# Kernel tuning notes

Hardware: AMD Instinct MI355X
Metric: run time of the kernel (lower is better)

The kernel has to match this reference:

```python
import jax, jax.numpy as jnp
import numpy as np

GAMMA = 0.5
K = 3
SKIP_THRESHOLD = 1.0


def setup_inputs() -> dict:
    key = jax.random.key(0)
    ks = jax.random.split(key, 11)
    in_dim, out_dim, mem_len = 1024, 128, 131072
    inp = {
        "x": jax.random.normal(ks[0], (1, in_dim), jnp.float32),
        "mean": jax.random.normal(ks[1], (in_dim,), jnp.float32),
        "std": jax.random.uniform(ks[2], (in_dim,), jnp.float32, 0.5, 1.5),
        "memory": jax.random.normal(ks[3], (mem_len, out_dim), jnp.float32),
        "mem_data": jax.random.normal(ks[4], (mem_len, in_dim), jnp.float32),
        "W_enc": jax.random.normal(ks[5], (in_dim, out_dim), jnp.float32) * 0.02,
        "b_enc": jnp.zeros((out_dim,), jnp.float32),
        "W_dec": jax.random.normal(ks[6], (out_dim, in_dim), jnp.float32) * 0.02,
        "b_dec": jnp.zeros((in_dim,), jnp.float32),
        "win_mean": jnp.zeros((), jnp.float32),   # WindowLoss running mean
        "win_std": jnp.ones((), jnp.float32),     # WindowLoss sample std (1 if population_std==0)
    }
    return inp


def reference(x, mean, std, memory, mem_data, W_enc, b_enc, W_dec, b_dec, win_mean, win_std):
    # normalize: new = (x - mean) / std, zero where std == 0
    new = jnp.where(std == 0, 0.0, (x - mean) / std)            # [1, in_dim]
    # encoder: Linear + Tanh
    enc = jnp.tanh(new @ W_enc + b_enc)                          # [1, out_dim]
    # window_loss: decoder reconstruction MSE, gated by ndtr of z-scored loss
    rec = enc @ W_dec + b_dec                                    # [1, in_dim]
    mse = jnp.mean((rec - new) ** 2)                             # scalar
    prob = jax.scipy.special.ndtr((mse - win_mean) / win_std)    # torch uses loss.item() -> constant
    win_loss = (SKIP_THRESHOLD - prob) / SKIP_THRESHOLD * mse
    # L1-distance top-k (smallest) against the memory bank
    dist = jnp.sum(jnp.abs(memory - enc), axis=1)                # [mem_len]
    neg_d, idx = jax.lax.top_k(-dist, K)
    distances = -neg_d                                           # [K] smallest distances
    expw = GAMMA ** jnp.arange(K, dtype=jnp.float32)
    loss_values = jnp.sum(distances * expw) / jnp.sum(expw)
    # conditional FIFO scatter update at the nearest index
    cond = loss_values <= win_loss
    i0 = idx[0]
    new_memory = jnp.where(cond, memory.at[i0].set(enc[0]), memory)
    new_mem_data = jnp.where(cond, mem_data.at[i0].set(x[0]), mem_data)
    loss_combined = win_loss + loss_values
    return loss_combined, new_memory, new_mem_data
```

## Files before the change

### kernel.cpp

```cpp
#include <hip/hip_runtime.h>
#include <math.h>
#include <float.h>

#define IN_DIM   1024
#define OUT_DIM  128
#define MEM_LEN  131072
#define DIST_BLOCKS 2048
#define COPY_BLOCKS 8192

#define NA_FLOATS  ((long long)MEM_LEN * OUT_DIM)
#define NB_FLOATS  ((long long)MEM_LEN * IN_DIM)
#define N_TOTAL    (NA_FLOATS + NB_FLOATS)
#define NA_CHUNKS  (NA_FLOATS / 4)
#define CMAX       ((N_TOTAL - 4) / 4)

__device__ __forceinline__ void ins3(float v, int i,
    float& v0, int& i0, float& v1, int& i1, float& v2, int& i2) {
  if (v < v0 || (v == v0 && i < i0)) {
    v2 = v1; i2 = i1; v1 = v0; i1 = i0; v0 = v; i0 = i;
  } else if (v < v1 || (v == v1 && i < i1)) {
    v2 = v1; i2 = i1; v1 = v; i1 = i;
  } else if (v < v2 || (v == v2 && i < i2)) {
    v2 = v; i2 = i;
  }
}

__global__ __launch_bounds__(1024) void k1_encode(
    const float* __restrict__ x, const float* __restrict__ mean,
    const float* __restrict__ stdv, const float* __restrict__ W_enc,
    const float* __restrict__ b_enc, const float* __restrict__ W_dec,
    const float* __restrict__ b_dec, const float* __restrict__ win_mean,
    const float* __restrict__ win_std,
    float* __restrict__ ws_enc, float* __restrict__ ws_winloss) {
  __shared__ float s_new[IN_DIM];
  __shared__ float s_part[8][OUT_DIM];
  __shared__ float s_enc[OUT_DIM];
  __shared__ float s_red[16];
  const int t = threadIdx.x;
  const float sd = stdv[t];
  const float nv = (sd == 0.0f) ? 0.0f : (x[t] - mean[t]) / sd;
  s_new[t] = nv;
  __syncthreads();
  const int o = t & (OUT_DIM - 1);
  const int p = t >> 7;
  float partial = 0.0f;
  #pragma unroll 8
  for (int i = 0; i < 128; ++i) {
    const int k = p * 128 + i;
    partial += s_new[k] * W_enc[k * OUT_DIM + o];
  }
  s_part[p][o] = partial;
  __syncthreads();
  if (t < OUT_DIM) {
    float sum = b_enc[t];
    #pragma unroll
    for (int pp = 0; pp < 8; ++pp) sum += s_part[pp][t];
    const float e = tanhf(sum);
    s_enc[t] = e;
    ws_enc[t] = e;
  }
  __syncthreads();
  float r = b_dec[t];
  #pragma unroll 8
  for (int k = 0; k < OUT_DIM; ++k) r += s_enc[k] * W_dec[k * IN_DIM + t];
  const float diff = r - nv;
  float sq = diff * diff;
  for (int off = 32; off; off >>= 1) sq += __shfl_xor(sq, off, 64);
  const int lane = t & 63, wid = t >> 6;
  if (lane == 0) s_red[wid] = sq;
  __syncthreads();
  if (t == 0) {
    float tot = 0.0f;
    #pragma unroll
    for (int w = 0; w < 16; ++w) tot += s_red[w];
    const float mse = tot / (float)IN_DIM;
    const float z = (mse - win_mean[0]) / win_std[0];
    const float prob = 0.5f * erfcf(-z * 0.70710678118654752440f);
    ws_winloss[0] = (1.0f - prob) * mse;
  }
}

__global__ __launch_bounds__(256) void k2_dist(
    const float* __restrict__ memory, const float* __restrict__ ws_enc,
    float* __restrict__ topv, int* __restrict__ topi) {
  const int t = threadIdx.x;
  const int lane = t & 63;
  const int wid = t >> 6;
  const int gw = blockIdx.x * 4 + wid;
  const float2 e = reinterpret_cast<const float2*>(ws_enc)[lane];
  float v0 = FLT_MAX, v1 = FLT_MAX, v2 = FLT_MAX;
  int i0 = 0x7fffffff, i1 = 0x7fffffff, i2 = 0x7fffffff;
  const int r0 = gw * 16;
  for (int rr = 0; rr < 16; ++rr) {
    const int r = r0 + rr;
    const float2 m = reinterpret_cast<const float2*>(memory)[(size_t)r * 64 + lane];
    float d = fabsf(m.x - e.x) + fabsf(m.y - e.y);
    for (int off = 32; off; off >>= 1) d += __shfl_xor(d, off, 64);
    ins3(d, r, v0, i0, v1, i1, v2, i2);
  }
  __shared__ float sv[4][3];
  __shared__ int   si[4][3];
  if (lane == 0) {
    sv[wid][0] = v0; sv[wid][1] = v1; sv[wid][2] = v2;
    si[wid][0] = i0; si[wid][1] = i1; si[wid][2] = i2;
  }
  __syncthreads();
  if (t == 0) {
    for (int w = 1; w < 4; ++w)
      for (int j = 0; j < 3; ++j)
        ins3(sv[w][j], si[w][j], v0, i0, v1, i1, v2, i2);
    topv[blockIdx.x * 3 + 0] = v0; topi[blockIdx.x * 3 + 0] = i0;
    topv[blockIdx.x * 3 + 1] = v1; topi[blockIdx.x * 3 + 1] = i1;
    topv[blockIdx.x * 3 + 2] = v2; topi[blockIdx.x * 3 + 2] = i2;
  }
}

__global__ __launch_bounds__(256) void copy_all(
    const float4* __restrict__ mem4, const float4* __restrict__ md4,
    float* __restrict__ out) {
  const int lane = threadIdx.x & 63;
  const int wid  = threadIdx.x >> 6;
  const long long wstride = (long long)gridDim.x * 4;
  const long long ngroups = (CMAX + 63) / 64;
  const float* memf = reinterpret_cast<const float*>(mem4);
  const float* mdf  = reinterpret_cast<const float*>(md4);
  for (long long g = (long long)blockIdx.x * 4 + wid; g < ngroups; g += wstride) {
    const long long c = 1 + g * 64 + lane;
    const bool valid = (c <= CMAX);
    float4 v = make_float4(0.f, 0.f, 0.f, 0.f);
    if (valid) v = (c < NA_CHUNKS) ? mem4[c] : md4[c - NA_CHUNKS];
    float aw = __shfl_up(v.w, 1, 64);
    if (lane == 0) {
      const long long s = 4 * c - 1;
      aw = (s < NA_FLOATS) ? memf[s] : mdf[s - NA_FLOATS];
    }
    if (valid) {
      const float4 o = make_float4(aw, v.x, v.y, v.z);
      *reinterpret_cast<float4*>(out + 4 * c) = o;
    }
  }
  if (blockIdx.x == 0 && threadIdx.x == 0) {
    out[1] = memf[0]; out[2] = memf[1]; out[3] = memf[2];
    out[N_TOTAL] = mdf[NB_FLOATS - 1];
  }
}

__global__ __launch_bounds__(1024) void k3_topk_update(
    const float* __restrict__ topv, const int* __restrict__ topi,
    const float* __restrict__ ws_winloss, const float* __restrict__ ws_enc,
    const float* __restrict__ x, float* __restrict__ out_loss,
    float* __restrict__ out_mem, float* __restrict__ out_md) {
  const int t = threadIdx.x;
  const int n = DIST_BLOCKS * 3;
  float v0 = FLT_MAX, v1 = FLT_MAX, v2 = FLT_MAX;
  int i0 = 0x7fffffff, i1 = 0x7fffffff, i2 = 0x7fffffff;
  for (int j = t; j < n; j += 1024) ins3(topv[j], topi[j], v0, i0, v1, i1, v2, i2);
  for (int off = 32; off; off >>= 1) {
    const float ov0 = __shfl_xor(v0, off, 64);
    const float ov1 = __shfl_xor(v1, off, 64);
    const float ov2 = __shfl_xor(v2, off, 64);
    const int oi0 = __shfl_xor(i0, off, 64);
    const int oi1 = __shfl_xor(i1, off, 64);
    const int oi2 = __shfl_xor(i2, off, 64);
    ins3(ov0, oi0, v0, i0, v1, i1, v2, i2);
    ins3(ov1, oi1, v0, i0, v1, i1, v2, i2);
    ins3(ov2, oi2, v0, i0, v1, i1, v2, i2);
  }
  __shared__ float sv[16][3];
  __shared__ int   si[16][3];
  __shared__ int s_i0, s_cond;
  const int lane = t & 63, wid = t >> 6;
  if (lane == 0) {
    sv[wid][0] = v0; sv[wid][1] = v1; sv[wid][2] = v2;
    si[wid][0] = i0; si[wid][1] = i1; si[wid][2] = i2;
  }
  __syncthreads();
  if (t == 0) {
    for (int w = 1; w < 16; ++w)
      for (int j = 0; j < 3; ++j)
        ins3(sv[w][j], si[w][j], v0, i0, v1, i1, v2, i2);
    const float loss_values = (v0 + 0.5f * v1 + 0.25f * v2) / 1.75f;
    const float wl = ws_winloss[0];
    out_loss[0] = wl + loss_values;
    s_i0 = i0;
    s_cond = (loss_values <= wl) ? 1 : 0;
  }
  __syncthreads();
  if (s_cond) {
    if (t < OUT_DIM) out_mem[(size_t)s_i0 * OUT_DIM + t] = ws_enc[t];
    out_md[(size_t)s_i0 * IN_DIM + t] = x[t];
  }
}

extern "C" void kernel_launch(void* const* d_in, const int* in_sizes, int n_in,
                              void* d_out, int out_size, void* d_ws, size_t ws_size,
                              hipStream_t stream) {
  const float* x        = (const float*)d_in[0];
  const float* mean     = (const float*)d_in[1];
  const float* stdv     = (const float*)d_in[2];
  const float* memory   = (const float*)d_in[3];
  const float* mem_data = (const float*)d_in[4];
  const float* W_enc    = (const float*)d_in[5];
  const float* b_enc    = (const float*)d_in[6];
  const float* W_dec    = (const float*)d_in[7];
  const float* b_dec    = (const float*)d_in[8];
  const float* win_mean = (const float*)d_in[9];
  const float* win_std  = (const float*)d_in[10];

  float* out      = (float*)d_out;
  float* out_loss = out;
  float* out_mem  = out + 1;
  float* out_md   = out + 1 + (size_t)MEM_LEN * OUT_DIM;

  float* ws        = (float*)d_ws;
  float* ws_enc    = ws;
  float* ws_wl     = ws + 128;
  float* ws_topv   = ws + 256;
  int*   ws_topi   = (int*)(ws + 256 + DIST_BLOCKS * 3);

  k1_encode<<<1, 1024, 0, stream>>>(x, mean, stdv, W_enc, b_enc, W_dec, b_dec,
                                    win_mean, win_std, ws_enc, ws_wl);
  k2_dist<<<DIST_BLOCKS, 256, 0, stream>>>(memory, ws_enc, ws_topv, ws_topi);
  copy_all<<<COPY_BLOCKS, 256, 0, stream>>>((const float4*)memory,
                                            (const float4*)mem_data, out);
  k3_topk_update<<<1, 1024, 0, stream>>>(ws_topv, ws_topi, ws_wl, ws_enc, x,
                                         out_loss, out_mem, out_md);
}
```

Baseline: 357.0 us.

## Fuse distance top-k into copy kernel and widen per-lane copy to four float4s

Merges the L1-distance/top-k kernel into the bulk output copy kernel. The first 2048 blocks compute partial top-3 before joining the grid-stride copy, which removes one launch and lets the memory reads of both phases overlap. The copy loop now handles four float4 chunks per lane with a fast path that avoids per-element bounds and source checks, and a slow path only for the group that straddles the two arrays and for the last group. This adds code complexity and makes the first blocks unbalanced relative to the rest.

```diff
diff --git a/kernel.cpp b/kernel.cpp
--- a/kernel.cpp
+++ b/kernel.cpp
@@ -5,14 +5,16 @@
 #define IN_DIM   1024
 #define OUT_DIM  128
 #define MEM_LEN  131072
+#define GRID     8192
 #define DIST_BLOCKS 2048
-#define COPY_BLOCKS 8192
 
 #define NA_FLOATS  ((long long)MEM_LEN * OUT_DIM)
 #define NB_FLOATS  ((long long)MEM_LEN * IN_DIM)
 #define N_TOTAL    (NA_FLOATS + NB_FLOATS)
 #define NA_CHUNKS  (NA_FLOATS / 4)
 #define CMAX       ((N_TOTAL - 4) / 4)
+#define NGROUPS    ((CMAX + 255) / 256)
+#define STRADDLE_G 16383
 
 __device__ __forceinline__ void ins3(float v, int i,
     float& v0, int& i0, float& v1, int& i1, float& v2, int& i2) {
@@ -80,68 +82,92 @@
   }
 }
 
-__global__ __launch_bounds__(256) void k2_dist(
-    const float* __restrict__ memory, const float* __restrict__ ws_enc,
+__global__ __launch_bounds__(256) void k2_fused(
+    const float* __restrict__ memory, const float* __restrict__ mem_data,
+    const float* __restrict__ ws_enc, float* __restrict__ out,
     float* __restrict__ topv, int* __restrict__ topi) {
   const int t = threadIdx.x;
   const int lane = t & 63;
-  const int wid = t >> 6;
-  const int gw = blockIdx.x * 4 + wid;
-  const float2 e = reinterpret_cast<const float2*>(ws_enc)[lane];
-  float v0 = FLT_MAX, v1 = FLT_MAX, v2 = FLT_MAX;
-  int i0 = 0x7fffffff, i1 = 0x7fffffff, i2 = 0x7fffffff;
-  const int r0 = gw * 16;
-  for (int rr = 0; rr < 16; ++rr) {
-    const int r = r0 + rr;
-    const float2 m = reinterpret_cast<const float2*>(memory)[(size_t)r * 64 + lane];
-    float d = fabsf(m.x - e.x) + fabsf(m.y - e.y);
-    for (int off = 32; off; off >>= 1) d += __shfl_xor(d, off, 64);
-    ins3(d, r, v0, i0, v1, i1, v2, i2);
-  }
-  __shared__ float sv[4][3];
-  __shared__ int   si[4][3];
-  if (lane == 0) {
-    sv[wid][0] = v0; sv[wid][1] = v1; sv[wid][2] = v2;
-    si[wid][0] = i0; si[wid][1] = i1; si[wid][2] = i2;
-  }
-  __syncthreads();
-  if (t == 0) {
-    for (int w = 1; w < 4; ++w)
-      for (int j = 0; j < 3; ++j)
-        ins3(sv[w][j], si[w][j], v0, i0, v1, i1, v2, i2);
-    topv[blockIdx.x * 3 + 0] = v0; topi[blockIdx.x * 3 + 0] = i0;
-    topv[blockIdx.x * 3 + 1] = v1; topi[blockIdx.x * 3 + 1] = i1;
-    topv[blockIdx.x * 3 + 2] = v2; topi[blockIdx.x * 3 + 2] = i2;
-  }
-}
-
-__global__ __launch_bounds__(256) void copy_all(
-    const float4* __restrict__ mem4, const float4* __restrict__ md4,
-    float* __restrict__ out) {
-  const int lane = threadIdx.x & 63;
-  const int wid  = threadIdx.x >> 6;
-  const long long wstride = (long long)gridDim.x * 4;
-  const long long ngroups = (CMAX + 63) / 64;
-  const float* memf = reinterpret_cast<const float*>(mem4);
-  const float* mdf  = reinterpret_cast<const float*>(md4);
-  for (long long g = (long long)blockIdx.x * 4 + wid; g < ngroups; g += wstride) {
-    const long long c = 1 + g * 64 + lane;
-    const bool valid = (c <= CMAX);
-    float4 v = make_float4(0.f, 0.f, 0.f, 0.f);
-    if (valid) v = (c < NA_CHUNKS) ? mem4[c] : md4[c - NA_CHUNKS];
-    float aw = __shfl_up(v.w, 1, 64);
+  const int wid  = t >> 6;
+  const float4* mem4 = reinterpret_cast<const float4*>(memory);
+  const float4* md4  = reinterpret_cast<const float4*>(mem_data);
+
+  if (blockIdx.x < DIST_BLOCKS) {
+    const float2 e = reinterpret_cast<const float2*>(ws_enc)[lane];
+    float v0 = FLT_MAX, v1 = FLT_MAX, v2 = FLT_MAX;
+    int i0 = 0x7fffffff, i1 = 0x7fffffff, i2 = 0x7fffffff;
+    const int r0 = (blockIdx.x * 4 + wid) * 16;
+    for (int rr = 0; rr < 16; ++rr) {
+      const int r = r0 + rr;
+      const float2 m = reinterpret_cast<const float2*>(memory)[(size_t)r * 64 + lane];
+      float d = fabsf(m.x - e.x) + fabsf(m.y - e.y);
+      for (int off = 32; off; off >>= 1) d += __shfl_xor(d, off, 64);
+      ins3(d, r, v0, i0, v1, i1, v2, i2);
+    }
+    __shared__ float sv[4][3];
+    __shared__ int   si[4][3];
     if (lane == 0) {
-      const long long s = 4 * c - 1;
-      aw = (s < NA_FLOATS) ? memf[s] : mdf[s - NA_FLOATS];
-    }
-    if (valid) {
-      const float4 o = make_float4(aw, v.x, v.y, v.z);
-      *reinterpret_cast<float4*>(out + 4 * c) = o;
-    }
-  }
-  if (blockIdx.x == 0 && threadIdx.x == 0) {
-    out[1] = memf[0]; out[2] = memf[1]; out[3] = memf[2];
-    out[N_TOTAL] = mdf[NB_FLOATS - 1];
+      sv[wid][0] = v0; sv[wid][1] = v1; sv[wid][2] = v2;
+      si[wid][0] = i0; si[wid][1] = i1; si[wid][2] = i2;
+    }
+    __syncthreads();
+    if (t == 0) {
+      for (int w = 1; w < 4; ++w)
+        for (int j = 0; j < 3; ++j)
+          ins3(sv[w][j], si[w][j], v0, i0, v1, i1, v2, i2);
+      topv[blockIdx.x * 3 + 0] = v0; topi[blockIdx.x * 3 + 0] = i0;
+      topv[blockIdx.x * 3 + 1] = v1; topi[blockIdx.x * 3 + 1] = i1;
+      topv[blockIdx.x * 3 + 2] = v2; topi[blockIdx.x * 3 + 2] = i2;
+    }
+  }
+
+  for (long long g = (long long)blockIdx.x * 4 + wid; g < NGROUPS;
+       g += (long long)GRID * 4) {
+    const long long b = g * 256 + (long long)lane * 4;
+    if (g != STRADDLE_G && g < NGROUPS - 1) {
+      const float4* src = (g < STRADDLE_G) ? mem4 : (md4 - NA_CHUNKS);
+      const float4 a0 = src[b + 1];
+      const float4 a1 = src[b + 2];
+      const float4 a2 = src[b + 3];
+      const float4 a3 = src[b + 4];
+      float prev = __shfl_up(a3.w, 1, 64);
+      if (lane == 0) {
+        const long long s = 1024LL * g + 3;
+        prev = (s < NA_FLOATS) ? memory[s] : mem_data[s - NA_FLOATS];
+      }
+      float4* o4 = reinterpret_cast<float4*>(out + 4 * b + 4);
+      o4[0] = make_float4(prev, a0.x, a0.y, a0.z);
+      o4[1] = make_float4(a0.w, a1.x, a1.y, a1.z);
+      o4[2] = make_float4(a1.w, a2.x, a2.y, a2.z);
+      o4[3] = make_float4(a2.w, a3.x, a3.y, a3.z);
+    } else {
+      float4 av[4];
+      #pragma unroll
+      for (int m = 0; m < 4; ++m) {
+        const long long c = b + 1 + m;
+        av[m] = (c <= CMAX)
+                  ? ((c < NA_CHUNKS) ? mem4[c] : md4[c - NA_CHUNKS])
+                  : make_float4(0.f, 0.f, 0.f, 0.f);
+      }
+      float prev = __shfl_up(av[3].w, 1, 64);
+      if (lane == 0) {
+        const long long s = 1024LL * g + 3;
+        prev = (s < NA_FLOATS) ? memory[s] : mem_data[s - NA_FLOATS];
+      }
+      float wprev = prev;
+      #pragma unroll
+      for (int m = 0; m < 4; ++m) {
+        const long long c = b + 1 + m;
+        if (c <= CMAX)
+          *reinterpret_cast<float4*>(out + 4 * c) =
+              make_float4(wprev, av[m].x, av[m].y, av[m].z);
+        wprev = av[m].w;
+      }
+    }
+  }
+  if (blockIdx.x == 0 && t == 0) {
+    out[1] = memory[0]; out[2] = memory[1]; out[3] = memory[2];
+    out[N_TOTAL] = mem_data[NB_FLOATS - 1];
   }
 }
 
@@ -220,9 +246,8 @@
 
   k1_encode<<<1, 1024, 0, stream>>>(x, mean, stdv, W_enc, b_enc, W_dec, b_dec,
                                     win_mean, win_std, ws_enc, ws_wl);
-  k2_dist<<<DIST_BLOCKS, 256, 0, stream>>>(memory, ws_enc, ws_topv, ws_topi);
-  copy_all<<<COPY_BLOCKS, 256, 0, stream>>>((const float4*)memory,
-                                            (const float4*)mem_data, out);
+  k2_fused<<<GRID, 256, 0, stream>>>(memory, mem_data, ws_enc, out,
+                                     ws_topv, ws_topi);
   k3_topk_update<<<1, 1024, 0, stream>>>(ws_topv, ws_topi, ws_wl, ws_enc, x,
                                          out_loss, out_mem, out_md);
 }
```

Result: slower. 424.0 us (+18.8%).
